# Performance work log

Measured on AMD Instinct MI355X. Metric: run time of the kernel, lower is better.

Reference implementation:

```python
import jax, jax.numpy as jnp
import numpy as np

B, T, F, U = 256, 512, 128, 1024  # batch, seq_len, feature dim, lstm units


def setup_inputs() -> dict:
    key = jax.random.key(0)
    ks = jax.random.split(key, 11)
    s = jnp.float32(0.05)  # small init so tanh/sigmoid stay in useful range
    f32 = jnp.float32
    return {
        "input_tensor": jax.random.normal(ks[0], (B, T, F), f32),
        # encoder LSTM weights (keras gate order i,f,c,o packed along last axis)
        "enc_Wx": jax.random.normal(ks[1], (F, 4 * U), f32) * s,
        "enc_Wh": jax.random.normal(ks[2], (U, 4 * U), f32) * s,
        "enc_b": jax.random.normal(ks[3], (4 * U,), f32) * s,
        # decoder LSTMCell weights (input dim = U, since it is fed its own output)
        "dec_Wx": jax.random.normal(ks[4], (U, 4 * U), f32) * s,
        "dec_Wh": jax.random.normal(ks[5], (U, 4 * U), f32) * s,
        "dec_b": jax.random.normal(ks[6], (4 * U,), f32) * s,
        # dense1: U -> U with relu; dense2: U -> F linear
        "d1_W": jax.random.normal(ks[7], (U, U), f32) * s,
        "d1_b": jax.random.normal(ks[8], (U,), f32) * s,
        "d2_W": jax.random.normal(ks[9], (U, F), f32) * s,
        "d2_b": jax.random.normal(ks[10], (F,), f32) * s,
    }


def _lstm_step(Wx, Wh, b):
    """Standard keras LSTM cell step. Gate packing order: i, f, g(cand), o."""
    def step(carry, x_t):
        h, c = carry
        z = x_t @ Wx + h @ Wh + b  # [B, 4U]
        i, f, g, o = jnp.split(z, 4, axis=-1)
        c = jax.nn.sigmoid(f) * c + jax.nn.sigmoid(i) * jnp.tanh(g)
        h = jax.nn.sigmoid(o) * jnp.tanh(c)
        return (h, c), h
    return step


def reference(input_tensor, enc_Wx, enc_Wh, enc_b, dec_Wx, dec_Wh, dec_b,
              d1_W, d1_b, d2_W, d2_b):
    x = input_tensor
    b_sz, t_len = x.shape[0], x.shape[1]
    u = enc_Wh.shape[0]
    h0 = jnp.zeros((b_sz, u), x.dtype)

    # Encoder: run LSTM over time, keep only final (h, c) (return_state=True).
    (h, c), _ = jax.lax.scan(_lstm_step(enc_Wx, enc_Wh, enc_b), (h0, h0),
                             jnp.swapaxes(x, 0, 1))  # xs: [T, B, F]

    # Decoder: feed previous output back as input, T steps.
    dec_step = _lstm_step(dec_Wx, dec_Wh, dec_b)
    def dec(carry, _):
        x_in, hh, cc = carry
        (hh, cc), _ = dec_step((hh, cc), x_in)
        return (hh, hh, cc), hh  # next input is the new hidden output

    _, hs = jax.lax.scan(dec, (h, h, c), None, length=t_len)  # hs: [T, B, U]

    # Per-step projections, fused over all timesteps (same math as in-loop dense).
    y = jnp.maximum(hs @ d1_W + d1_b, 0.0) @ d2_W + d2_b  # [T, B, F]
    return jnp.swapaxes(y, 0, 1)  # [B, T, F]
```

## Files before the change

### kernel.cpp

```cpp
#include <hip/hip_runtime.h>
#include <hip/hip_bf16.h>
#include <math.h>
#include <stdio.h>


typedef __attribute__((ext_vector_type(8))) short short8;
typedef __attribute__((ext_vector_type(4))) float f32x4;

#define MFMA(a, b, c) __builtin_amdgcn_mfma_f32_16x16x32_bf16(a, b, c, 0, 0, 0)

#define SEG_STEPS 8
#define RING_SLOTS 9

__device__ __forceinline__ short f2bf(float f) {
  union { __hip_bfloat16 h; short s; } u;
  u.h = __float2bfloat16(f);
  return u.s;
}
__device__ __forceinline__ void split3(float x, short& a, short& b, short& c) {
  union { __hip_bfloat16 h; short s; } u;
  u.h = __float2bfloat16(x); a = u.s;
  float r1 = x - __bfloat162float(u.h);
  u.h = __float2bfloat16(r1); b = u.s;
  float r2 = r1 - __bfloat162float(u.h);
  u.h = __float2bfloat16(r2); c = u.s;
}
__device__ __forceinline__ float sigm(float x) { return 1.0f / (1.0f + expf(-x)); }

__global__ void pack_w(const float* __restrict__ a, const float* __restrict__ b,
                       short8* __restrict__ dst, int KC, int mode, int ncols,
                       int limbs) {
  int gid = blockIdx.x * 256 + threadIdx.x;
  int lane = gid & 63;
  int kc = (gid >> 6) % KC;
  int nt = gid / (KC * 64);
  int u16 = lane & 15, kq = lane >> 4;
  int kbase = kc * 32 + kq * 8;
  int col;
  if (mode <= 1) { int g = nt & 3, ub = nt >> 2; col = g * 1024 + ub * 16 + u16; }
  else col = nt * 16 + u16;
  short8 v0, v1, v2;
#pragma unroll
  for (int j = 0; j < 8; ++j) {
    int k = kbase + j;
    float x;
    if (mode == 0)      x = a[(size_t)k * 4096 + col] + b[(size_t)k * 4096 + col];
    else if (mode == 1) x = (k < 1024) ? a[(size_t)k * 4096 + col]
                                       : b[(size_t)(k - 1024) * 4096 + col];
    else                x = a[(size_t)k * ncols + col];
    short sa, sb, sc; split3(x, sa, sb, sc);
    v0[j] = sa; v1[j] = sb; v2[j] = sc;
  }
  if (limbs == 3) {
    size_t base = (size_t)(nt * KC + kc) * 3 * 64 + lane;
    dst[base] = v0; dst[base + 64] = v1; dst[base + 128] = v2;
  } else {
    dst[(size_t)(nt * KC + kc) * 64 + lane] = v0;
  }
}

__global__ void pack_x32(const float* __restrict__ src, short8* __restrict__ dst,
                         int t0) {
  int gid = blockIdx.x * 256 + threadIdx.x;
  int lane = gid & 63;
  int kx = (gid >> 6) & 3;
  int mt = (gid >> 8) & 15;
  int tloc = gid >> 12;
  int bb = mt * 16 + (lane & 15);
  int fb = kx * 32 + (lane >> 4) * 8;
  const float* s = src + ((size_t)bb * 512 + (t0 + tloc)) * 128 + fb;
  short8 v0, v1, v2;
#pragma unroll
  for (int j = 0; j < 8; ++j) {
    short sa, sb, sc; split3(s[j], sa, sb, sc);
    v0[j] = sa; v1[j] = sb; v2[j] = sc;
  }
  size_t base = (size_t)((tloc * 16 + mt) * 4 + kx) * 3 * 64 + lane;
  dst[base] = v0; dst[base + 64] = v1; dst[base + 128] = v2;
}

__global__ void zero_f(float* p, int n) {
  int i = blockIdx.x * 256 + threadIdx.x;
  if (i < n) p[i] = 0.f;
}

template<int KCT>
__global__ __launch_bounds__(512) void lstm_seg(
    const short8* __restrict__ Ax, const short8* __restrict__ W,
    const float* __restrict__ bias, float* __restrict__ cst,
    short8* __restrict__ ring, short8* __restrict__ Hring,
    int gstep, unsigned* __restrict__ bar) {
  constexpr int NJ = KCT / 2;
  int tid = threadIdx.x;
  int lane = tid & 63, wv = tid >> 6;
  int wr = wv & 1, wc = wv >> 1;
  int wkcin = wv >> 2, wmtl = wv & 3;
  int xcd = blockIdx.x & 7, idx = blockIdx.x >> 3;
  int mb = idx & 3, ub = xcd * 8 + (idx >> 2);
  int u16 = lane & 15, quad = lane >> 4;
  const size_t H3R = (size_t)16 * 32 * 3 * 64;
  const size_t XT  = (size_t)16 * 4 * 3 * 64;
  const size_t HR  = (size_t)16 * 32 * 64;
  __shared__ short8 stg[3][2][4][3][64];
  __shared__ float zt[64][68];
  __shared__ __align__(16) short hb[64][48];
  float bv = bias[wc * 1024 + ub * 16 + u16];
  unsigned* cnt = bar + mb;
  unsigned* gen = bar + 4 + mb;
  int smt = mb * 4 + wmtl;

  for (int i = 0; i < SEG_STEPS; ++i) {
    int t = gstep + i;
    const short8* slotR = ring + (size_t)(t % RING_SLOTS) * H3R;
    short8* slotW = ring + (size_t)((t + 1) % RING_SLOTS) * H3R;
    const short8* Axs = (KCT == 36) ? (Ax + (size_t)(t & 31) * XT) : nullptr;
    auto asrc = [&](int kc) -> const short8* {
      if (KCT == 36 && kc >= 32)
        return Axs + ((size_t)(smt * 4 + (kc - 32)) * 3) * 64 + lane;
      return slotR + ((size_t)(smt * 32 + kc) * 3) * 64 + lane;
    };
    {
      const short8* p = asrc(wkcin);
      short8 w0 = p[0], w1 = p[64], w2 = p[128];
      short8* d = &stg[0][wkcin][wmtl][0][lane];
      d[0] = w0; d[64] = w1; d[128] = w2;
    }
    short8 rA0, rA1, rA2;
    { const short8* p = asrc(2 + wkcin); rA0 = p[0]; rA1 = p[64]; rA2 = p[128]; }
    const f32x4 z4 = {0.f, 0.f, 0.f, 0.f};
    f32x4 acc0 = z4, acc1 = z4;
    const short8* Bp = W + ((size_t)(ub * 4 + wc) * KCT) * 3 * 64 + lane;
    asm volatile("s_waitcnt lgkmcnt(0)" ::: "memory");
    __builtin_amdgcn_s_barrier();
    asm volatile("" ::: "memory");
    int bsel = 0;
    for (int j = 0; j < NJ; ++j) {
      int bnext = bsel + 1; if (bnext == 3) bnext = 0;
      if (j + 1 < NJ) {
        short8* d = &stg[bnext][wkcin][wmtl][0][lane];
        d[0] = rA0; d[64] = rA1; d[128] = rA2;
      }
      if (j + 2 < NJ) {
        const short8* p = asrc(2 * (j + 2) + wkcin);
        rA0 = p[0]; rA1 = p[64]; rA2 = p[128];
      }
      asm volatile("s_waitcnt lgkmcnt(0)" ::: "memory");
      __builtin_amdgcn_s_barrier();
      asm volatile("" ::: "memory");
#pragma unroll
      for (int kcin = 0; kcin < 2; ++kcin) {
        short8 b0 = Bp[0], b1 = Bp[64], b2 = Bp[128];
        Bp += 192;
        short8 x0 = stg[bsel][kcin][2 * wr + 0][0][lane];
        short8 x1 = stg[bsel][kcin][2 * wr + 0][1][lane];
        short8 x2 = stg[bsel][kcin][2 * wr + 0][2][lane];
        short8 y0 = stg[bsel][kcin][2 * wr + 1][0][lane];
        short8 y1 = stg[bsel][kcin][2 * wr + 1][1][lane];
        short8 y2 = stg[bsel][kcin][2 * wr + 1][2][lane];
        acc0 = MFMA(x0, b0, acc0);  acc1 = MFMA(y0, b0, acc1);
        acc0 = MFMA(x0, b1, acc0);  acc1 = MFMA(y0, b1, acc1);
        acc0 = MFMA(x1, b0, acc0);  acc1 = MFMA(y1, b0, acc1);
        acc0 = MFMA(x1, b1, acc0);  acc1 = MFMA(y1, b1, acc1);
        acc0 = MFMA(x0, b2, acc0);  acc1 = MFMA(y0, b2, acc1);
        acc0 = MFMA(x2, b0, acc0);  acc1 = MFMA(y2, b0, acc1);
      }
      bsel = bnext;
    }

#pragma unroll
    for (int r = 0; r < 4; ++r) {
      zt[(2 * wr + 0) * 16 + quad * 4 + r][wc * 16 + u16] = acc0[r] + bv;
      zt[(2 * wr + 1) * 16 + quad * 4 + r][wc * 16 + u16] = acc1[r] + bv;
    }
    __syncthreads();

    {
      int r = tid >> 3, up = tid & 7;
      int m = mb * 64 + r;
      float2* cp2 = (float2*)(cst + (size_t)m * 1024 + ub * 16) + up;
      float2 cv = *cp2;
#pragma unroll
      for (int jj = 0; jj < 2; ++jj) {
        int uu = up * 2 + jj;
        float iv = zt[r][uu];
        float fv = zt[r][16 + uu];
        float gv = zt[r][32 + uu];
        float ov = zt[r][48 + uu];
        float cin = jj ? cv.y : cv.x;
        float cn = sigm(fv) * cin + sigm(iv) * tanhf(gv);
        if (jj) cv.y = cn; else cv.x = cn;
        float hval = sigm(ov) * tanhf(cn);
        short sa, sb, sc; split3(hval, sa, sb, sc);
        hb[r][uu] = sa; hb[r][16 + uu] = sb; hb[r][32 + uu] = sc;
      }
      *cp2 = cv;
    }
    __syncthreads();

    if (tid < 128) {
      int r = tid >> 1, s = tid & 1;
      int m = mb * 64 + r;
      int ubase = ub * 16 + s * 8;
      short8 h0 = *(const short8*)&hb[r][s * 8];
      short8 h1 = *(const short8*)&hb[r][16 + s * 8];
      short8 h2 = *(const short8*)&hb[r][32 + s * 8];
      int mtw = m >> 4, r16 = m & 15;
      int kcw = ubase >> 5, ko = ubase & 31;
      int lane_t = r16 + 16 * (ko >> 3);
      size_t base = ((size_t)(mtw * 32 + kcw) * 3) * 64 + lane_t;
      slotW[base] = h0; slotW[base + 64] = h1; slotW[base + 128] = h2;
      if (Hring)
        Hring[(size_t)i * HR + (size_t)(mtw * 32 + kcw) * 64 + lane_t] = h0;
    }
    __syncthreads();

    if (i + 1 < SEG_STEPS) {
      if (tid == 0) {
        unsigned tick = (unsigned)(t + 1);
        unsigned old = __hip_atomic_fetch_add(cnt, 1u, __ATOMIC_RELEASE,
                                              __HIP_MEMORY_SCOPE_AGENT);
        if (old == 63u) {
          __hip_atomic_store(cnt, 0u, __ATOMIC_RELAXED,
                             __HIP_MEMORY_SCOPE_AGENT);
          __hip_atomic_store(gen, tick, __ATOMIC_RELEASE,
                             __HIP_MEMORY_SCOPE_AGENT);
        } else {
          while (__hip_atomic_load(gen, __ATOMIC_RELAXED,
                                   __HIP_MEMORY_SCOPE_AGENT) < tick)
            __builtin_amdgcn_s_sleep(2);
        }
      }
      __syncthreads();
      asm volatile("" ::: "memory");
    }
  }
}

__global__ __launch_bounds__(256) void proj(
    const short8* __restrict__ HS, const short8* __restrict__ W1,
    const float* __restrict__ b1, const short8* __restrict__ W2,
    const float* __restrict__ b2, float* __restrict__ out, int t0) {
  int tid = threadIdx.x;
  int lane = tid & 63, wv = tid >> 6;
  int wr = wv & 1, wc = wv >> 1;
  int tloc = blockIdx.x >> 2, mb = blockIdx.x & 3;
  int t = t0 + tloc;
  const short8* A = HS + (size_t)tloc * 16 * 32 * 64;
  int u16 = lane & 15, quad = lane >> 4;
  int mt0 = mb * 4 + wr * 2;
  __shared__ short a1f[4][8][512];
  const f32x4 z4 = {0.f, 0.f, 0.f, 0.f};
  f32x4 acc2[2][4];
#pragma unroll
  for (int i = 0; i < 2; ++i)
#pragma unroll
    for (int jj = 0; jj < 4; ++jj) acc2[i][jj] = z4;

  for (int q = 0; q < 4; ++q) {
    f32x4 acc1[2][8];
#pragma unroll
    for (int i = 0; i < 2; ++i)
#pragma unroll
      for (int n = 0; n < 8; ++n) acc1[i][n] = z4;
    for (int kc = 0; kc < 32; ++kc) {
      short8 av0 = A[(size_t)(mt0 * 32 + kc) * 64 + lane];
      short8 av1 = A[(size_t)((mt0 + 1) * 32 + kc) * 64 + lane];
#pragma unroll
      for (int n = 0; n < 8; ++n) {
        int nt = q * 16 + wc * 8 + n;
        short8 bv = W1[(size_t)(nt * 32 + kc) * 64 + lane];
        acc1[0][n] = MFMA(av0, bv, acc1[0][n]);
        acc1[1][n] = MFMA(av1, bv, acc1[1][n]);
      }
    }
    __syncthreads();
#pragma unroll
    for (int i = 0; i < 2; ++i)
#pragma unroll
      for (int n = 0; n < 8; ++n)
#pragma unroll
        for (int r = 0; r < 4; ++r) {
          int rl = wr * 32 + i * 16 + quad * 4 + r;
          int nloc = wc * 128 + n * 16 + u16;
          float v = fmaxf(acc1[i][n][r] + b1[q * 256 + nloc], 0.f);
          int mtl = rl >> 4, r16 = rl & 15;
          int kcl = nloc >> 5, ko = nloc & 31;
          a1f[mtl][kcl][(r16 + 16 * (ko >> 3)) * 8 + (ko & 7)] = f2bf(v);
        }
    __syncthreads();
    for (int kcl = 0; kcl < 8; ++kcl) {
      short8 av0 = *(const short8*)&a1f[wr * 2 + 0][kcl][lane * 8];
      short8 av1 = *(const short8*)&a1f[wr * 2 + 1][kcl][lane * 8];
#pragma unroll
      for (int jj = 0; jj < 4; ++jj) {
        int nt2 = wc * 4 + jj;
        short8 bv = W2[(size_t)(nt2 * 32 + q * 8 + kcl) * 64 + lane];
        acc2[0][jj] = MFMA(av0, bv, acc2[0][jj]);
        acc2[1][jj] = MFMA(av1, bv, acc2[1][jj]);
      }
    }
  }
#pragma unroll
  for (int i = 0; i < 2; ++i)
#pragma unroll
    for (int jj = 0; jj < 4; ++jj)
#pragma unroll
      for (int r = 0; r < 4; ++r) {
        int rl = wr * 32 + i * 16 + quad * 4 + r;
        int f = wc * 64 + jj * 16 + u16;
        int bb = mb * 64 + rl;
        out[((size_t)bb * 512 + t) * 128 + f] = acc2[i][jj][r] + b2[f];
      }
}

static void launch_seg(const void* fn, void** args, hipStream_t stream) {
  hipError_t e = hipLaunchCooperativeKernel(fn, dim3(256), dim3(512), args, 0,
                                            stream);
  if (e != hipSuccess) {
    fprintf(stderr, "coop launch failed (%s); falling back to plain launch\n",
            hipGetErrorString(e));
    hipLaunchKernel(fn, dim3(256), dim3(512), args, 0, stream);
  }
}

extern "C" void kernel_launch(void* const* d_in, const int* in_sizes, int n_in,
                              void* d_out, int out_size, void* d_ws, size_t ws_size,
                              hipStream_t stream) {
  const float* x     = (const float*)d_in[0];
  const float* encWx = (const float*)d_in[1];
  const float* encWh = (const float*)d_in[2];
  const float* encb  = (const float*)d_in[3];
  const float* decWx = (const float*)d_in[4];
  const float* decWh = (const float*)d_in[5];
  const float* decb  = (const float*)d_in[6];
  const float* d1W   = (const float*)d_in[7];
  const float* d1b   = (const float*)d_in[8];
  const float* d2W   = (const float*)d_in[9];
  const float* d2b   = (const float*)d_in[10];

  char* ws = (char*)d_ws;
  size_t off = 0;
  short8* Wenc = (short8*)(ws + off); off += (size_t)256 * 36 * 3 * 64 * 16;
  short8* Wdec = (short8*)(ws + off); off += (size_t)256 * 32 * 3 * 64 * 16;
  short8* W1   = (short8*)(ws + off); off += (size_t)64 * 32 * 64 * 16;
  short8* W2   = (short8*)(ws + off); off += (size_t)8 * 32 * 64 * 16;
  short8* Xr   = (short8*)(ws + off); off += (size_t)32 * 16 * 4 * 3 * 64 * 16;
  short8* ring = (short8*)(ws + off); off += (size_t)RING_SLOTS * 16 * 32 * 3 * 64 * 16;
  short8* Hring= (short8*)(ws + off); off += (size_t)32 * 16 * 32 * 64 * 16;
  float*  cst  = (float*)(ws + off);  off += (size_t)256 * 1024 * 4;
  unsigned* bar = (unsigned*)(ws + off); off += 256;
  (void)in_sizes; (void)n_in; (void)out_size;
  if (ws_size < off) {
    fprintf(stderr, "kernel_launch: ws_size=%zu < needed=%zu -- aborting launch\n",
            ws_size, off);
    return;
  }

  pack_w<<<2304, 256, 0, stream>>>(encWh, encWx, Wenc, 36, 1, 4096, 3);
  pack_w<<<2048, 256, 0, stream>>>(decWx, decWh, Wdec, 32, 0, 4096, 3);
  pack_w<<<512, 256, 0, stream>>>(d1W, nullptr, W1, 32, 2, 1024, 1);
  pack_w<<<64, 256, 0, stream>>>(d2W, nullptr, W2, 32, 3, 128, 1);
  zero_f<<<1536, 256, 0, stream>>>((float*)ring, 16 * 32 * 3 * 64 * 8);
  zero_f<<<1024, 256, 0, stream>>>(cst, 256 * 1024);
  zero_f<<<1, 256, 0, stream>>>((float*)bar, 8);

  const size_t HR = (size_t)16 * 32 * 64;

  for (int c = 0; c < 16; ++c) {
    pack_x32<<<512, 256, 0, stream>>>(x, Xr, c * 32);
    for (int k = 0; k < 4; ++k) {
      const short8* axp = Xr; const short8* wp = Wenc; const float* bp = encb;
      float* cp = cst; short8* rp = ring; short8* hrp = nullptr;
      int gs = c * 32 + k * 8; unsigned* barp = bar;
      void* args[] = {&axp, &wp, &bp, &cp, &rp, &hrp, &gs, &barp};
      launch_seg((const void*)lstm_seg<36>, args, stream);
    }
  }
  for (int c = 0; c < 16; ++c) {
    for (int k = 0; k < 4; ++k) {
      const short8* axp = nullptr; const short8* wp = Wdec; const float* bp = decb;
      float* cp = cst; short8* rp = ring;
      short8* hrp = Hring + (size_t)(k * 8) * HR;
      int gs = 512 + c * 32 + k * 8; unsigned* barp = bar;
      void* args[] = {&axp, &wp, &bp, &cp, &rp, &hrp, &gs, &barp};
      launch_seg((const void*)lstm_seg<32>, args, stream);
    }
    proj<<<128, 256, 0, stream>>>(Hring, W1, d1b, W2, d2b, (float*)d_out, c * 32);
  }
}
```

Baseline: 45.38 ms.

## Store recurrent state as fp32, split to bf16 limbs in-kernel, lengthen segments

The persistent LSTM kernel now runs 32 timesteps per launch instead of 8, so there are four times fewer cooperative launches. The hidden-state ring and the x buffer now hold fp32 instead of pre-split 3-limb bf16, which cuts ring traffic from 48 to 32 bytes per 8 values. The three-way bf16 split moves into the consumer's LDS staging path. The weight B loads are double-buffered in registers across the K loop. The grid barrier uses monotonic tick counters instead of resetting, and the encoder/decoder weight buffers share one allocation. The cost is extra split arithmetic in every consumer block and a ring of 33 slots.

```diff
diff --git a/kernel.cpp b/kernel.cpp
--- a/kernel.cpp
+++ b/kernel.cpp
@@ -9,8 +9,9 @@
 
 #define MFMA(a, b, c) __builtin_amdgcn_mfma_f32_16x16x32_bf16(a, b, c, 0, 0, 0)
 
-#define SEG_STEPS 8
-#define RING_SLOTS 9
+#define SEG_STEPS 32
+#define RING_SLOTS 33
+#define SLOT_F4 65536
 
 __device__ __forceinline__ short f2bf(float f) {
   union { __hip_bfloat16 h; short s; } u;
@@ -26,6 +27,16 @@
   u.h = __float2bfloat16(r2); c = u.s;
 }
 __device__ __forceinline__ float sigm(float x) { return 1.0f / (1.0f + expf(-x)); }
+
+__device__ __forceinline__ void split8(const f32x4& a, const f32x4& b,
+                                       short8& v0, short8& v1, short8& v2) {
+  float ff[8] = {a.x, a.y, a.z, a.w, b.x, b.y, b.z, b.w};
+#pragma unroll
+  for (int jj = 0; jj < 8; ++jj) {
+    short sa, sb, sc; split3(ff[jj], sa, sb, sc);
+    v0[jj] = sa; v1[jj] = sb; v2[jj] = sc;
+  }
+}
 
 __global__ void pack_w(const float* __restrict__ a, const float* __restrict__ b,
                        short8* __restrict__ dst, int KC, int mode, int ncols,
@@ -59,8 +70,8 @@
   }
 }
 
-__global__ void pack_x32(const float* __restrict__ src, short8* __restrict__ dst,
-                         int t0) {
+__global__ void pack_x32f(const float* __restrict__ src, f32x4* __restrict__ dst,
+                          int t0) {
   int gid = blockIdx.x * 256 + threadIdx.x;
   int lane = gid & 63;
   int kx = (gid >> 6) & 3;
@@ -69,14 +80,10 @@
   int bb = mt * 16 + (lane & 15);
   int fb = kx * 32 + (lane >> 4) * 8;
   const float* s = src + ((size_t)bb * 512 + (t0 + tloc)) * 128 + fb;
-  short8 v0, v1, v2;
-#pragma unroll
-  for (int j = 0; j < 8; ++j) {
-    short sa, sb, sc; split3(s[j], sa, sb, sc);
-    v0[j] = sa; v1[j] = sb; v2[j] = sc;
-  }
-  size_t base = (size_t)((tloc * 16 + mt) * 4 + kx) * 3 * 64 + lane;
-  dst[base] = v0; dst[base + 64] = v1; dst[base + 128] = v2;
+  f32x4 a = *(const f32x4*)s;
+  f32x4 b = *(const f32x4*)(s + 4);
+  size_t base = ((size_t)((tloc * 16 + mt) * 4 + kx) * 64 + lane) * 2;
+  dst[base] = a; dst[base + 1] = b;
 }
 
 __global__ void zero_f(float* p, int n) {
@@ -86,9 +93,9 @@
 
 template<int KCT>
 __global__ __launch_bounds__(512) void lstm_seg(
-    const short8* __restrict__ Ax, const short8* __restrict__ W,
+    const f32x4* __restrict__ Xr4, const short8* __restrict__ W,
     const float* __restrict__ bias, float* __restrict__ cst,
-    short8* __restrict__ ring, short8* __restrict__ Hring,
+    f32x4* __restrict__ ring4, short8* __restrict__ Hring,
     int gstep, unsigned* __restrict__ bar) {
   constexpr int NJ = KCT / 2;
   int tid = threadIdx.x;
@@ -98,73 +105,101 @@
   int xcd = blockIdx.x & 7, idx = blockIdx.x >> 3;
   int mb = idx & 3, ub = xcd * 8 + (idx >> 2);
   int u16 = lane & 15, quad = lane >> 4;
-  const size_t H3R = (size_t)16 * 32 * 3 * 64;
-  const size_t XT  = (size_t)16 * 4 * 3 * 64;
-  const size_t HR  = (size_t)16 * 32 * 64;
-  __shared__ short8 stg[3][2][4][3][64];
+  int smt = mb * 4 + wmtl;
+  const size_t HR = (size_t)16 * 32 * 64;
+
+  __shared__ short8 Abuf[3][2][4][3][64];
   __shared__ float zt[64][68];
-  __shared__ __align__(16) short hb[64][48];
+  __shared__ __align__(16) float hbf[64][20];
+
   float bv = bias[wc * 1024 + ub * 16 + u16];
   unsigned* cnt = bar + mb;
   unsigned* gen = bar + 4 + mb;
-  int smt = mb * 4 + wmtl;
+  unsigned ebase = (unsigned)(gstep >> 5) * 31u;
+  const short8* Wb = W + ((size_t)(ub * 4 + wc) * KCT) * 3 * 64 + lane;
+
+#define LOADB(P, B00, B01, B02, B10, B11, B12) do {                     \
+    const short8* bq_ = Wb + (size_t)(P) * 384;                         \
+    B00 = bq_[0];   B01 = bq_[64];  B02 = bq_[128];                     \
+    B10 = bq_[192]; B11 = bq_[256]; B12 = bq_[320]; } while (0)
+
+#define LOADRA(P) do {                                                  \
+    int kc0_ = 2 * (P) + wkcin;                                         \
+    const f32x4* sp_;                                                   \
+    if (KCT == 36 && kc0_ >= 32)                                        \
+      sp_ = Xr4 + ((((size_t)(t & 31) * 16 + smt) * 4 + (kc0_ - 32)) * 64 + lane) * 2; \
+    else                                                                \
+      sp_ = ringR4 + (((size_t)(smt * 32 + kc0_)) * 64 + lane) * 2;     \
+    rA0 = __builtin_nontemporal_load(sp_);                              \
+    rA1 = __builtin_nontemporal_load(sp_ + 1); } while (0)
+
+#define WRITEA(BW) do {                                                 \
+    short8 v0_, v1_, v2_;                                               \
+    split8(rA0, rA1, v0_, v1_, v2_);                                    \
+    short8* d_ = &Abuf[BW][wkcin][wmtl][0][lane];                       \
+    d_[0] = v0_; d_[64] = v1_; d_[128] = v2_; } while (0)
+
+#define BARSYNC() do {                                                  \
+    asm volatile("s_waitcnt lgkmcnt(0)" ::: "memory");                  \
+    __builtin_amdgcn_s_barrier();                                       \
+    asm volatile("" ::: "memory"); } while (0)
+
+#define COMPUTE(BJ, B00, B01, B02, B10, B11, B12) do {                  \
+    short8 x0 = Abuf[BJ][0][2 * wr + 0][0][lane];                       \
+    short8 x1 = Abuf[BJ][0][2 * wr + 0][1][lane];                       \
+    short8 x2 = Abuf[BJ][0][2 * wr + 0][2][lane];                       \
+    short8 y0 = Abuf[BJ][0][2 * wr + 1][0][lane];                       \
+    short8 y1 = Abuf[BJ][0][2 * wr + 1][1][lane];                       \
+    short8 y2 = Abuf[BJ][0][2 * wr + 1][2][lane];                       \
+    acc0 = MFMA(x0, B00, acc0);  acc1 = MFMA(y0, B00, acc1);            \
+    acc0 = MFMA(x0, B01, acc0);  acc1 = MFMA(y0, B01, acc1);            \
+    acc0 = MFMA(x1, B00, acc0);  acc1 = MFMA(y1, B00, acc1);            \
+    acc0 = MFMA(x1, B01, acc0);  acc1 = MFMA(y1, B01, acc1);            \
+    acc0 = MFMA(x0, B02, acc0);  acc1 = MFMA(y0, B02, acc1);            \
+    acc0 = MFMA(x2, B00, acc0);  acc1 = MFMA(y2, B00, acc1);            \
+    x0 = Abuf[BJ][1][2 * wr + 0][0][lane];                              \
+    x1 = Abuf[BJ][1][2 * wr + 0][1][lane];                              \
+    x2 = Abuf[BJ][1][2 * wr + 0][2][lane];                              \
+    y0 = Abuf[BJ][1][2 * wr + 1][0][lane];                              \
+    y1 = Abuf[BJ][1][2 * wr + 1][1][lane];                              \
+    y2 = Abuf[BJ][1][2 * wr + 1][2][lane];                              \
+    acc0 = MFMA(x0, B10, acc0);  acc1 = MFMA(y0, B10, acc1);            \
+    acc0 = MFMA(x0, B11, acc0);  acc1 = MFMA(y0, B11, acc1);            \
+    acc0 = MFMA(x1, B10, acc0);  acc1 = MFMA(y1, B10, acc1);            \
+    acc0 = MFMA(x1, B11, acc0);  acc1 = MFMA(y1, B11, acc1);            \
+    acc0 = MFMA(x0, B12, acc0);  acc1 = MFMA(y0, B12, acc1);            \
+    acc0 = MFMA(x2, B10, acc0);  acc1 = MFMA(y2, B10, acc1); } while (0)
 
   for (int i = 0; i < SEG_STEPS; ++i) {
     int t = gstep + i;
-    const short8* slotR = ring + (size_t)(t % RING_SLOTS) * H3R;
-    short8* slotW = ring + (size_t)((t + 1) % RING_SLOTS) * H3R;
-    const short8* Axs = (KCT == 36) ? (Ax + (size_t)(t & 31) * XT) : nullptr;
-    auto asrc = [&](int kc) -> const short8* {
-      if (KCT == 36 && kc >= 32)
-        return Axs + ((size_t)(smt * 4 + (kc - 32)) * 3) * 64 + lane;
-      return slotR + ((size_t)(smt * 32 + kc) * 3) * 64 + lane;
-    };
-    {
-      const short8* p = asrc(wkcin);
-      short8 w0 = p[0], w1 = p[64], w2 = p[128];
-      short8* d = &stg[0][wkcin][wmtl][0][lane];
-      d[0] = w0; d[64] = w1; d[128] = w2;
-    }
-    short8 rA0, rA1, rA2;
-    { const short8* p = asrc(2 + wkcin); rA0 = p[0]; rA1 = p[64]; rA2 = p[128]; }
-    const f32x4 z4 = {0.f, 0.f, 0.f, 0.f};
-    f32x4 acc0 = z4, acc1 = z4;
-    const short8* Bp = W + ((size_t)(ub * 4 + wc) * KCT) * 3 * 64 + lane;
-    asm volatile("s_waitcnt lgkmcnt(0)" ::: "memory");
-    __builtin_amdgcn_s_barrier();
-    asm volatile("" ::: "memory");
-    int bsel = 0;
-    for (int j = 0; j < NJ; ++j) {
-      int bnext = bsel + 1; if (bnext == 3) bnext = 0;
-      if (j + 1 < NJ) {
-        short8* d = &stg[bnext][wkcin][wmtl][0][lane];
-        d[0] = rA0; d[64] = rA1; d[128] = rA2;
-      }
-      if (j + 2 < NJ) {
-        const short8* p = asrc(2 * (j + 2) + wkcin);
-        rA0 = p[0]; rA1 = p[64]; rA2 = p[128];
-      }
-      asm volatile("s_waitcnt lgkmcnt(0)" ::: "memory");
-      __builtin_amdgcn_s_barrier();
-      asm volatile("" ::: "memory");
-#pragma unroll
-      for (int kcin = 0; kcin < 2; ++kcin) {
-        short8 b0 = Bp[0], b1 = Bp[64], b2 = Bp[128];
-        Bp += 192;
-        short8 x0 = stg[bsel][kcin][2 * wr + 0][0][lane];
-        short8 x1 = stg[bsel][kcin][2 * wr + 0][1][lane];
-        short8 x2 = stg[bsel][kcin][2 * wr + 0][2][lane];
-        short8 y0 = stg[bsel][kcin][2 * wr + 1][0][lane];
-        short8 y1 = stg[bsel][kcin][2 * wr + 1][1][lane];
-        short8 y2 = stg[bsel][kcin][2 * wr + 1][2][lane];
-        acc0 = MFMA(x0, b0, acc0);  acc1 = MFMA(y0, b0, acc1);
-        acc0 = MFMA(x0, b1, acc0);  acc1 = MFMA(y0, b1, acc1);
-        acc0 = MFMA(x1, b0, acc0);  acc1 = MFMA(y1, b0, acc1);
-        acc0 = MFMA(x1, b1, acc0);  acc1 = MFMA(y1, b1, acc1);
-        acc0 = MFMA(x0, b2, acc0);  acc1 = MFMA(y0, b2, acc1);
-        acc0 = MFMA(x2, b0, acc0);  acc1 = MFMA(y2, b0, acc1);
-      }
-      bsel = bnext;
+    const f32x4* ringR4 = ring4 + (size_t)(t % RING_SLOTS) * SLOT_F4;
+    f32x4* ringW4 = ring4 + (size_t)((t + 1) % RING_SLOTS) * SLOT_F4;
+    const f32x4 zf4 = {0.f, 0.f, 0.f, 0.f};
+    f32x4 acc0 = {0.f, 0.f, 0.f, 0.f}, acc1 = {0.f, 0.f, 0.f, 0.f};
+    (void)zf4;
+    f32x4 rA0, rA1;
+    short8 p00, p01, p02, p10, p11, p12;
+    short8 q00, q01, q02, q10, q11, q12;
+
+    LOADRA(0);
+    LOADB(0, p00, p01, p02, p10, p11, p12);
+    WRITEA(0);
+    LOADRA(1);
+
+    for (int m2 = 0; m2 < NJ / 2; ++m2) {
+      int j0 = 2 * m2, j1 = 2 * m2 + 1;
+      WRITEA((j0 + 1) % 3);
+      if (m2 < NJ / 2 - 1) LOADRA(j0 + 2);
+      LOADB(j0 + 1, q00, q01, q02, q10, q11, q12);
+      BARSYNC();
+      COMPUTE(j0 % 3, p00, p01, p02, p10, p11, p12);
+      if (m2 < NJ / 2 - 1) {
+        WRITEA((j1 + 1) % 3);
+        LOADRA(j1 + 2);
+        LOADB(j1 + 1, p00, p01, p02, p10, p11, p12);
+      }
+      BARSYNC();
+      COMPUTE(j1 % 3, q00, q01, q02, q10, q11, q12);
     }
 
 #pragma unroll
@@ -189,9 +224,7 @@
         float cin = jj ? cv.y : cv.x;
         float cn = sigm(fv) * cin + sigm(iv) * tanhf(gv);
         if (jj) cv.y = cn; else cv.x = cn;
-        float hval = sigm(ov) * tanhf(cn);
-        short sa, sb, sc; split3(hval, sa, sb, sc);
-        hb[r][uu] = sa; hb[r][16 + uu] = sb; hb[r][32 + uu] = sc;
+        hbf[r][uu] = sigm(ov) * tanhf(cn);
       }
       *cp2 = cv;
     }
@@ -201,39 +234,55 @@
       int r = tid >> 1, s = tid & 1;
       int m = mb * 64 + r;
       int ubase = ub * 16 + s * 8;
-      short8 h0 = *(const short8*)&hb[r][s * 8];
-      short8 h1 = *(const short8*)&hb[r][16 + s * 8];
-      short8 h2 = *(const short8*)&hb[r][32 + s * 8];
+      const float* hp = &hbf[r][s * 8];
+      f32x4 h4a = *(const f32x4*)hp;
+      f32x4 h4b = *(const f32x4*)(hp + 4);
       int mtw = m >> 4, r16 = m & 15;
       int kcw = ubase >> 5, ko = ubase & 31;
       int lane_t = r16 + 16 * (ko >> 3);
-      size_t base = ((size_t)(mtw * 32 + kcw) * 3) * 64 + lane_t;
-      slotW[base] = h0; slotW[base + 64] = h1; slotW[base + 128] = h2;
-      if (Hring)
-        Hring[(size_t)i * HR + (size_t)(mtw * 32 + kcw) * 64 + lane_t] = h0;
-    }
-    __syncthreads();
+      size_t idx = ((size_t)(mtw * 32 + kcw) * 64 + lane_t);
+      __builtin_nontemporal_store(h4a, ringW4 + idx * 2);
+      __builtin_nontemporal_store(h4b, ringW4 + idx * 2 + 1);
+      if (Hring) {
+        short8 h0;
+#pragma unroll
+        for (int jj = 0; jj < 8; ++jj) h0[jj] = f2bf(hp[jj]);
+        __builtin_nontemporal_store(h0, Hring + (size_t)i * HR + idx);
+      }
+    }
 
     if (i + 1 < SEG_STEPS) {
+      __syncthreads();
       if (tid == 0) {
-        unsigned tick = (unsigned)(t + 1);
+        unsigned tick = ebase + (unsigned)i + 1u;
         unsigned old = __hip_atomic_fetch_add(cnt, 1u, __ATOMIC_RELEASE,
                                               __HIP_MEMORY_SCOPE_AGENT);
-        if (old == 63u) {
-          __hip_atomic_store(cnt, 0u, __ATOMIC_RELAXED,
-                             __HIP_MEMORY_SCOPE_AGENT);
+        if (old == 64u * tick - 1u) {
           __hip_atomic_store(gen, tick, __ATOMIC_RELEASE,
                              __HIP_MEMORY_SCOPE_AGENT);
         } else {
-          while (__hip_atomic_load(gen, __ATOMIC_RELAXED,
-                                   __HIP_MEMORY_SCOPE_AGENT) < tick)
-            __builtin_amdgcn_s_sleep(2);
+          unsigned v = 0;
+          do {
+            for (int ph = 0; ph < 8; ++ph) {
+              v = __hip_atomic_load(gen, __ATOMIC_RELAXED,
+                                    __HIP_MEMORY_SCOPE_AGENT);
+              if (v >= tick) break;
+              __builtin_amdgcn_s_sleep(1);
+            }
+            if (v < tick)
+              v = __hip_atomic_fetch_add(gen, 0u, __ATOMIC_RELAXED,
+                                         __HIP_MEMORY_SCOPE_AGENT);
+          } while (v < tick);
         }
       }
       __syncthreads();
-      asm volatile("" ::: "memory");
-    }
-  }
+    }
+  }
+#undef LOADB
+#undef LOADRA
+#undef WRITEA
+#undef BARSYNC
+#undef COMPUTE
 }
 
 __global__ __launch_bounds__(256) void proj(
@@ -340,12 +389,11 @@
 
   char* ws = (char*)d_ws;
   size_t off = 0;
-  short8* Wenc = (short8*)(ws + off); off += (size_t)256 * 36 * 3 * 64 * 16;
-  short8* Wdec = (short8*)(ws + off); off += (size_t)256 * 32 * 3 * 64 * 16;
+  short8* Wrec = (short8*)(ws + off); off += (size_t)256 * 36 * 3 * 64 * 16;
   short8* W1   = (short8*)(ws + off); off += (size_t)64 * 32 * 64 * 16;
   short8* W2   = (short8*)(ws + off); off += (size_t)8 * 32 * 64 * 16;
-  short8* Xr   = (short8*)(ws + off); off += (size_t)32 * 16 * 4 * 3 * 64 * 16;
-  short8* ring = (short8*)(ws + off); off += (size_t)RING_SLOTS * 16 * 32 * 3 * 64 * 16;
+  f32x4*  Xr   = (f32x4*)(ws + off);  off += (size_t)32 * 16 * 4 * 64 * 32;
+  f32x4*  ring = (f32x4*)(ws + off);  off += (size_t)RING_SLOTS * SLOT_F4 * 16;
   short8* Hring= (short8*)(ws + off); off += (size_t)32 * 16 * 32 * 64 * 16;
   float*  cst  = (float*)(ws + off);  off += (size_t)256 * 1024 * 4;
   unsigned* bar = (unsigned*)(ws + off); off += 256;
@@ -356,35 +404,30 @@
     return;
   }
 
-  pack_w<<<2304, 256, 0, stream>>>(encWh, encWx, Wenc, 36, 1, 4096, 3);
-  pack_w<<<2048, 256, 0, stream>>>(decWx, decWh, Wdec, 32, 0, 4096, 3);
+  pack_w<<<2304, 256, 0, stream>>>(encWh, encWx, Wrec, 36, 1, 4096, 3);
   pack_w<<<512, 256, 0, stream>>>(d1W, nullptr, W1, 32, 2, 1024, 1);
   pack_w<<<64, 256, 0, stream>>>(d2W, nullptr, W2, 32, 3, 128, 1);
-  zero_f<<<1536, 256, 0, stream>>>((float*)ring, 16 * 32 * 3 * 64 * 8);
+  zero_f<<<1024, 256, 0, stream>>>((float*)ring, 256 * 1024);
   zero_f<<<1024, 256, 0, stream>>>(cst, 256 * 1024);
   zero_f<<<1, 256, 0, stream>>>((float*)bar, 8);
 
   const size_t HR = (size_t)16 * 32 * 64;
 
   for (int c = 0; c < 16; ++c) {
-    pack_x32<<<512, 256, 0, stream>>>(x, Xr, c * 32);
-    for (int k = 0; k < 4; ++k) {
-      const short8* axp = Xr; const short8* wp = Wenc; const float* bp = encb;
-      float* cp = cst; short8* rp = ring; short8* hrp = nullptr;
-      int gs = c * 32 + k * 8; unsigned* barp = bar;
-      void* args[] = {&axp, &wp, &bp, &cp, &rp, &hrp, &gs, &barp};
-      launch_seg((const void*)lstm_seg<36>, args, stream);
-    }
-  }
+    pack_x32f<<<512, 256, 0, stream>>>(x, Xr, c * 32);
+    const f32x4* axp = Xr; const short8* wp = Wrec; const float* bp = encb;
+    float* cp = cst; f32x4* rp = ring; short8* hrp = nullptr;
+    int gs = c * 32; unsigned* barp = bar;
+    void* args[] = {&axp, &wp, &bp, &cp, &rp, &hrp, &gs, &barp};
+    launch_seg((const void*)lstm_seg<36>, args, stream);
+  }
+  pack_w<<<2048, 256, 0, stream>>>(decWx, decWh, Wrec, 32, 0, 4096, 3);
   for (int c = 0; c < 16; ++c) {
-    for (int k = 0; k < 4; ++k) {
-      const short8* axp = nullptr; const short8* wp = Wdec; const float* bp = decb;
-      float* cp = cst; short8* rp = ring;
-      short8* hrp = Hring + (size_t)(k * 8) * HR;
-      int gs = 512 + c * 32 + k * 8; unsigned* barp = bar;
-      void* args[] = {&axp, &wp, &bp, &cp, &rp, &hrp, &gs, &barp};
-      launch_seg((const void*)lstm_seg<32>, args, stream);
-    }
+    const f32x4* axp = nullptr; const short8* wp = Wrec; const float* bp = decb;
+    float* cp = cst; f32x4* rp = ring; short8* hrp = Hring;
+    int gs = 512 + c * 32; unsigned* barp = bar;
+    void* args[] = {&axp, &wp, &bp, &cp, &rp, &hrp, &gs, &barp};
+    launch_seg((const void*)lstm_seg<32>, args, stream);
     proj<<<128, 256, 0, stream>>>(Hring, W1, d1b, W2, d2b, (float*)d_out, c * 32);
   }
 }
```

New measurement: 38.88 ms. 1.17x faster.
